# Optimization experiments

Hardware: AMD Instinct MI355X
Metric: run time of the kernel (lower is better)

Reference implementation:

```python
import jax, jax.numpy as jnp
import numpy as np


def conv1d(x, w, b):
    # x: [B, C_in, T], w: [C_out, C_in, K] (torch layout), b: [C_out]
    y = jax.lax.conv_general_dilated(
        x, w, window_strides=(1,), padding='SAME',
        dimension_numbers=('NCH', 'OIH', 'NCH'))
    return y + b[None, :, None]


def setup_inputs() -> dict:
    B, T, IN, H, D, K = 16, 2048, 80, 512, 512, 1024
    key = jax.random.key(0)
    ks = jax.random.split(key, 10)
    f32 = jnp.float32

    def w_init(k, shape, fan_in):
        return (jax.random.normal(k, shape, f32) / np.sqrt(fan_in)).astype(f32)

    return {
        'mels':    jax.random.normal(ks[0], (B, T, IN), f32),
        'enc_w1':  w_init(ks[1], (H, IN, 3), IN * 3),
        'enc_b1':  jnp.zeros((H,), f32),
        'enc_w2':  w_init(ks[2], (D, H, 3), H * 3),
        'enc_b2':  jnp.zeros((D,), f32),
        'codebook': jax.random.normal(ks[3], (K, D), f32),
        'dec_w1':  w_init(ks[4], (H, D, 3), D * 3),
        'dec_b1':  jnp.zeros((H,), f32),
        'dec_w2':  w_init(ks[5], (IN, H, 3), H * 3),
        'dec_b2':  jnp.zeros((IN,), f32),
    }


def reference(mels, enc_w1, enc_b1, enc_w2, enc_b2, codebook,
              dec_w1, dec_b1, dec_w2, dec_b2):
    B, T, _ = mels.shape
    D = codebook.shape[1]

    # ---- encoder: conv -> relu -> conv ----
    x = jnp.swapaxes(mels, 1, 2)                      # [B, in_dim, T]
    z = conv1d(jax.nn.relu(conv1d(x, enc_w1, enc_b1)), enc_w2, enc_b2)  # [B, D, T]

    # ---- vector quantization ----
    z_t = jnp.swapaxes(z, 1, 2)                       # [B, T, D]
    flat = z_t.reshape(-1, D)                         # [B*T, D]
    d = ((flat ** 2).sum(axis=1, keepdims=True)
         - 2.0 * flat @ codebook.T
         + (codebook ** 2).sum(axis=1)[None, :])      # [B*T, K]
    idx = jnp.argmin(d, axis=1).reshape(B, T)         # [B, T] int
    quantized = codebook[idx]                         # [B, T, D] gather

    # ---- decoder: conv -> relu -> conv ----
    q = jnp.swapaxes(quantized, 1, 2)                 # [B, D, T]
    recon = conv1d(jax.nn.relu(conv1d(q, dec_w1, dec_b1)), dec_w2, dec_b2)
    recon = jnp.swapaxes(recon, 1, 2)                 # [B, T, in_dim]
    return recon, idx
```

## Files before the change

### kernel.cpp

```cpp
#include <hip/hip_runtime.h>
#include <hip/hip_bf16.h>

#define Bsz   16
#define Tn    2048
#define INC   80
#define Hc    512
#define Dc    512
#define NCODE 1024
#define BT    (Bsz * Tn)
#define RECON_N (Bsz * Tn * INC)
#define MARGIN 0.03f

typedef __attribute__((ext_vector_type(8))) short bf16x8;
typedef __attribute__((ext_vector_type(4))) float f32x4;
typedef __attribute__((ext_vector_type(4))) unsigned short u16x4;

static __device__ __forceinline__ unsigned short f2bf(float x) {
    unsigned u = __float_as_uint(x);
    u += 0x7FFF + ((u >> 16) & 1);
    return (unsigned short)(u >> 16);
}
static __device__ __forceinline__ float bf2f(unsigned short h) {
    return __uint_as_float((unsigned)h << 16);
}

typedef const __attribute__((address_space(1))) unsigned int* gas_p;
typedef __attribute__((address_space(3))) unsigned int* las_p;
static __device__ __forceinline__ void async16(const void* g, const void* l) {
    __builtin_amdgcn_global_load_lds(
        (gas_p)(unsigned long long)g,
        (las_p)(unsigned int)(unsigned long long)l,
        16, 0, 0);
}

__global__ __launch_bounds__(64)
void code_norms(const float* __restrict__ CB, float* __restrict__ CN) {
    int j = blockIdx.x;
    int lane = threadIdx.x;
    const float4* row = (const float4*)(CB + (size_t)j * Dc);
    float s = 0.f;
    #pragma unroll
    for (int i = 0; i < 2; ++i) {
        float4 v = row[lane + i * 64];
        s = fmaf(v.x, v.x, s);
        s = fmaf(v.y, v.y, s);
        s = fmaf(v.z, v.z, s);
        s = fmaf(v.w, v.w, s);
    }
    #pragma unroll
    for (int off = 32; off > 0; off >>= 1) s += __shfl_down(s, off, 64);
    if (lane == 0) CN[j] = s;
}

__global__ __launch_bounds__(256)
void cb_transpose(const float* __restrict__ CB, float* __restrict__ CBt) {
    const int j0 = blockIdx.x * 64;
    const int d0 = blockIdx.y * 64;
    __shared__ float ts[64][65];
    const int tid = threadIdx.x;
    for (int i = tid; i < 4096; i += 256) {
        int r = i >> 6, c = i & 63;
        ts[r][c] = CB[(size_t)(j0 + r) * Dc + d0 + c];
    }
    __syncthreads();
    for (int i = tid; i < 4096; i += 256) {
        int r = i >> 6, c = i & 63;
        CBt[(size_t)(d0 + r) * NCODE + j0 + c] = ts[c][r];
    }
}

__global__ __launch_bounds__(256)
void mels_transpose(const float* __restrict__ M, float* __restrict__ MT) {
    const int t0 = blockIdx.x * 64;
    const int b  = blockIdx.y;
    __shared__ float ts[64][84];
    const int tid = threadIdx.x;
    #pragma unroll
    for (int it = 0; it < 5; ++it) {
        int i = tid + it * 256;
        int t = i / 20, c4 = i % 20;
        *(float4*)&ts[t][c4 * 4] =
            *(const float4*)&M[((size_t)b * Tn + t0 + t) * INC + c4 * 4];
    }
    __syncthreads();
    #pragma unroll
    for (int it = 0; it < 20; ++it) {
        int i = tid + it * 256;
        int c = i >> 6, t = i & 63;
        MT[((size_t)b * INC + c) * Tn + t0 + t] = ts[t][c];
    }
}

__global__ __launch_bounds__(256)
void wt_transpose(const float* __restrict__ W, float* __restrict__ Wt,
                  int Cin, int Cout) {
    const int o0 = blockIdx.x * 64;
    const int c0 = blockIdx.y * 16;
    __shared__ float ts[48][65];
    const int tid = threadIdx.x;
    for (int i = tid; i < 64 * 48; i += 256) {
        int o = i / 48, ck = i % 48;
        int oo = o0 + o;
        float v = 0.f;
        if (oo < Cout) v = W[(size_t)oo * Cin * 3 + c0 * 3 + ck];
        ts[ck][o] = v;
    }
    __syncthreads();
    for (int i = tid; i < 48 * 64; i += 256) {
        int o = i & 63, ck = i >> 6;
        int oo = o0 + o;
        if (oo < Cout) Wt[(size_t)(c0 * 3 + ck) * Cout + oo] = ts[ck][o];
    }
}

__global__ __launch_bounds__(256)
void wsplit(const float* __restrict__ W, unsigned short* __restrict__ Whl) {
    int o = blockIdx.x, k = blockIdx.y;
    #pragma unroll
    for (int it = 0; it < 2; ++it) {
        int c = threadIdx.x + it * 256;
        float v = W[((size_t)o * Hc + c) * 3 + k];
        unsigned short h = f2bf(v);
        size_t base = ((size_t)(k * Hc + o) * 16 + (c >> 5)) * 64 + (c & 31);
        Whl[base] = h;
        Whl[base + 32] = f2bf(v - bf2f(h));
    }
}

__global__ __launch_bounds__(256)
void wsplit80(const float* __restrict__ W, unsigned short* __restrict__ Wh) {
    int o = blockIdx.x, k = blockIdx.y;
    #pragma unroll
    for (int it = 0; it < 2; ++it) {
        int c = threadIdx.x + it * 256;
        Wh[((size_t)k * INC + o) * Hc + c] = f2bf(W[((size_t)o * Hc + c) * 3 + k]);
    }
}

__global__ __launch_bounds__(256)
void cbsplit(const float* __restrict__ CB, unsigned short* __restrict__ CBhl) {
    int j = blockIdx.x;
    #pragma unroll
    for (int it = 0; it < 2; ++it) {
        int d = threadIdx.x + it * 256;
        float v = CB[(size_t)j * Dc + d];
        unsigned short h = f2bf(v);
        size_t base = ((size_t)j * 16 + (d >> 5)) * 64 + (d & 31);
        CBhl[base] = h;
        CBhl[base + 32] = f2bf(v - bf2f(h));
    }
}

__global__ __launch_bounds__(256)
void conv_enc1(const float* __restrict__ X, const float* __restrict__ Wt,
               const float* __restrict__ bias, unsigned short* __restrict__ Yhl) {
    const int t0 = blockIdx.x * 64;
    const int o0 = blockIdx.y * 128;
    const int b  = blockIdx.z;
    union SharedU {
        struct { float Xs[16][72]; float Ws[48][132]; } a;
        float Ys[128][69];
    };
    __shared__ __align__(16) SharedU su;
    float (&Xs)[16][72]  = su.a.Xs;
    float (&Ws)[48][132] = su.a.Ws;
    const int tid = threadIdx.x;
    const int tx = tid & 15, ty = tid >> 4;
    float acc[8][4] = {};
    const float* Xb = X + (size_t)b * INC * Tn;

    for (int c0 = 0; c0 < INC; c0 += 16) {
        for (int i = tid; i < 16 * 66; i += 256) {
            int cc = i / 66, tt = i % 66;
            int t = t0 + tt - 1;
            float v = 0.f;
            if (t >= 0 && t < Tn) v = Xb[(size_t)(c0 + cc) * Tn + t];
            Xs[cc][tt] = v;
        }
        for (int i = tid; i < 48 * 128; i += 256) {
            int o = i & 127, ck = i >> 7;
            Ws[ck][o] = Wt[(size_t)(c0 * 3 + ck) * Hc + o0 + o];
        }
        __syncthreads();
        #pragma unroll
        for (int cc = 0; cc < 16; ++cc) {
            float4 xa = *(const float4*)&Xs[cc][tx * 4];
            float2 xb2 = *(const float2*)&Xs[cc][tx * 4 + 4];
            float xv[6] = {xa.x, xa.y, xa.z, xa.w, xb2.x, xb2.y};
            #pragma unroll
            for (int k = 0; k < 3; ++k) {
                float4 wa = *(const float4*)&Ws[cc * 3 + k][ty * 4];
                float4 wb = *(const float4*)&Ws[cc * 3 + k][64 + ty * 4];
                float wv[8] = {wa.x, wa.y, wa.z, wa.w, wb.x, wb.y, wb.z, wb.w};
                #pragma unroll
                for (int i8 = 0; i8 < 8; ++i8)
                    #pragma unroll
                    for (int j = 0; j < 4; ++j)
                        acc[i8][j] = fmaf(wv[i8], xv[k + j], acc[i8][j]);
            }
        }
        __syncthreads();
    }
    #pragma unroll
    for (int og = 0; og < 2; ++og)
        #pragma unroll
        for (int oi = 0; oi < 4; ++oi) {
            int ol = og * 64 + ty * 4 + oi;
            float bv = bias[o0 + ol];
            const int i8 = og * 4 + oi;
            #pragma unroll
            for (int j = 0; j < 4; ++j)
                su.Ys[ol][tx * 4 + j] = fmaxf(acc[i8][j] + bv, 0.f);
        }
    __syncthreads();
    #pragma unroll
    for (int it = 0; it < 8; ++it) {
        int i = tid + it * 256;
        int oq = i & 31, t = i >> 5;
        int o4 = o0 + oq * 4;
        u16x4 h, l;
        #pragma unroll
        for (int r = 0; r < 4; ++r) {
            float v = su.Ys[oq * 4 + r][t];
            unsigned short hh = f2bf(v);
            h[r] = hh;
            l[r] = f2bf(v - bf2f(hh));
        }
        size_t base = ((size_t)(b * (Tn + 2) + 1 + t0 + t) * 16 + (o4 >> 5)) * 64
                      + (o4 & 31);
        *(u16x4*)(Yhl + base) = h;
        *(u16x4*)(Yhl + base + 32) = l;
    }
}

__global__ __launch_bounds__(256)
void zero_guards(unsigned short* __restrict__ Yhl) {
    const int b = blockIdx.x;
    u16x4 z = {0, 0, 0, 0};
    size_t r0 = (size_t)(b * (Tn + 2)) * 1024;
    size_t r1 = (size_t)(b * (Tn + 2) + Tn + 1) * 1024;
    *(u16x4*)(Yhl + r0 + threadIdx.x * 4) = z;
    *(u16x4*)(Yhl + r1 + threadIdx.x * 4) = z;
}

__global__ __launch_bounds__(256)
void zero_guards512(unsigned short* __restrict__ Y) {
    const int b = blockIdx.x;
    u16x4 z = {0, 0, 0, 0};
    size_t r0 = (size_t)(b * (Tn + 2)) * 512;
    size_t r1 = (size_t)(b * (Tn + 2) + Tn + 1) * 512;
    if (threadIdx.x < 128) {
        *(u16x4*)(Y + r0 + threadIdx.x * 4) = z;
        *(u16x4*)(Y + r1 + threadIdx.x * 4) = z;
    }
}

__global__ __launch_bounds__(256)
void split_t(const float* __restrict__ X, unsigned short* __restrict__ Yhl,
             int rowStride, int rowOff) {
    const int t0 = blockIdx.x * 64;
    const int c0 = blockIdx.y * 64;
    const int b  = blockIdx.z;
    __shared__ __align__(16) float ts[64][68];
    const int tid = threadIdx.x;
    #pragma unroll
    for (int it = 0; it < 4; ++it) {
        int i = tid + it * 256;
        int cc = i >> 4, t4 = i & 15;
        float4 v = *(const float4*)&X[((size_t)b * Hc + c0 + cc) * Tn + t0 + t4 * 4];
        ts[t4 * 4 + 0][cc] = v.x;
        ts[t4 * 4 + 1][cc] = v.y;
        ts[t4 * 4 + 2][cc] = v.z;
        ts[t4 * 4 + 3][cc] = v.w;
    }
    __syncthreads();
    #pragma unroll
    for (int it = 0; it < 4; ++it) {
        int i = tid + it * 256;
        int t = i >> 4, c4 = i & 15;
        int c = c0 + c4 * 4;
        float4 v = *(const float4*)&ts[t][c4 * 4];
        float va[4] = {v.x, v.y, v.z, v.w};
        u16x4 h, l;
        #pragma unroll
        for (int r = 0; r < 4; ++r) {
            unsigned short hh = f2bf(va[r]);
            h[r] = hh;
            l[r] = f2bf(va[r] - bf2f(hh));
        }
        size_t base = ((size_t)(b * rowStride + rowOff + t0 + t) * 16 + (c >> 5)) * 64
                      + (c & 31);
        *(u16x4*)(Yhl + base) = h;
        *(u16x4*)(Yhl + base + 32) = l;
    }
}

__global__ __launch_bounds__(256)
void conv_mid_mfma(const unsigned short* __restrict__ Xhl,
                   const unsigned short* __restrict__ Whl,
                   const float* __restrict__ bias,
                   float* __restrict__ Y) {
    const int lin  = blockIdx.x + (blockIdx.y << 4) + (blockIdx.z << 6);
    const int slot = lin >> 3;
    const int b  = ((lin & 7) << 1) | (slot >> 6);
    const int t0 = ((slot & 63) >> 2) << 7;
    const int o0 = (slot & 3) << 7;
    __shared__ __align__(16) unsigned short XL[2][136 * 64];
    const int tid  = threadIdx.x;
    const int lane = tid & 63;
    const int wave = tid >> 6;
    const int wm = wave >> 1, wn = wave & 1;
    const int m16 = lane & 15;
    const int q = lane >> 4;
    const int lrow = lane >> 3;
    const int lchk = (lane & 7) ^ lrow;
    const unsigned short* Xb = Xhl + ((size_t)b * (Tn + 2) + t0) * 1024
                               + (size_t)lrow * 1024 + lchk * 8;

    f32x4 acc[4][4];
    #pragma unroll
    for (int mt = 0; mt < 4; ++mt)
        #pragma unroll
        for (int nt = 0; nt < 4; ++nt)
            acc[mt][nt] = (f32x4){0.f, 0.f, 0.f, 0.f};

    #pragma unroll
    for (int i = 0; i < 5; ++i) {
        int ii = wave + i * 4;
        if (ii < 17)
            async16(Xb + (size_t)ii * 8192, &XL[0][ii * 512]);
    }

    for (int c0 = 0; c0 < Hc; c0 += 32) {
        const int buf = (c0 >> 5) & 1;
        __syncthreads();
        if (c0 + 32 < Hc) {
            const unsigned short* src = Xb + (size_t)((c0 >> 5) + 1) * 64;
            #pragma unroll
            for (int i = 0; i < 5; ++i) {
                int ii = wave + i * 4;
                if (ii < 17)
                    async16(src + (size_t)ii * 8192, &XL[buf ^ 1][ii * 512]);
            }
        }
        #pragma unroll
        for (int k = 0; k < 3; ++k) {
            bf16x8 Ah[4], Al[4];
            #pragma unroll
            for (int mt = 0; mt < 4; ++mt) {
                int o = o0 + wm * 64 + mt * 16 + m16;
                size_t base = ((size_t)(k * Hc + o) * 16 + (c0 >> 5)) * 64 + q * 8;
                Ah[mt] = *(const bf16x8*)(Whl + base);
                Al[mt] = *(const bf16x8*)(Whl + base + 32);
            }
            #pragma unroll
            for (int nt = 0; nt < 4; ++nt) {
                int row = wn * 64 + nt * 16 + m16 + k;
                const unsigned short* rp = &XL[buf][row * 64];
                int ph = (q ^ (row & 7)) * 8;
                union { bf16x8 v; uint4 u; } bh, bl;
                bh.u = *(const uint4*)(rp + ph);
                bl.u = *(const uint4*)(rp + (ph ^ 32));
                __builtin_amdgcn_s_setprio(1);
                #pragma unroll
                for (int mt = 0; mt < 4; ++mt)
                    acc[mt][nt] = __builtin_amdgcn_mfma_f32_16x16x32_bf16(
                        Ah[mt], bh.v, acc[mt][nt], 0, 0, 0);
                #pragma unroll
                for (int mt = 0; mt < 4; ++mt)
                    acc[mt][nt] = __builtin_amdgcn_mfma_f32_16x16x32_bf16(
                        Al[mt], bh.v, acc[mt][nt], 0, 0, 0);
                #pragma unroll
                for (int mt = 0; mt < 4; ++mt)
                    acc[mt][nt] = __builtin_amdgcn_mfma_f32_16x16x32_bf16(
                        Ah[mt], bl.v, acc[mt][nt], 0, 0, 0);
                __builtin_amdgcn_s_setprio(0);
            }
        }
    }
    float* Yb = Y + (size_t)b * Hc * Tn;
    #pragma unroll
    for (int mt = 0; mt < 4; ++mt) {
        int ob = o0 + wm * 64 + mt * 16 + q * 4;
        float4 bq = *(const float4*)&bias[ob];
        float bqa[4] = {bq.x, bq.y, bq.z, bq.w};
        #pragma unroll
        for (int nt = 0; nt < 4; ++nt) {
            int t = t0 + wn * 64 + nt * 16 + m16;
            #pragma unroll
            for (int r = 0; r < 4; ++r)
                Yb[(size_t)(ob + r) * Tn + t] = acc[mt][nt][r] + bqa[r];
        }
    }
}

__global__ __launch_bounds__(256)
void dec2_mfma(const unsigned short* __restrict__ Xt,
               const unsigned short* __restrict__ Wh2,
               const float* __restrict__ bias, float* __restrict__ OUT) {
    const int t0 = blockIdx.x * 128;
    const int b  = blockIdx.z;
    __shared__ __align__(16) unsigned short XL[2][136 * 64];
    const int tid = threadIdx.x;
    const int lane = tid & 63;
    const int wave = tid >> 6;
    const int wn = wave;
    const int m16 = lane & 15;
    const int q = lane >> 4;
    const int lrow = lane >> 3;
    const int lchk = (lane & 7) ^ lrow;
    const unsigned short* Xb = Xt + ((size_t)b * (Tn + 2) + t0) * 512
                               + (size_t)lrow * 512 + lchk * 8;

    f32x4 acc[5][2];
    #pragma unroll
    for (int mt = 0; mt < 5; ++mt)
        #pragma unroll
        for (int nt = 0; nt < 2; ++nt)
            acc[mt][nt] = (f32x4){0.f, 0.f, 0.f, 0.f};

    #pragma unroll
    for (int i = 0; i < 5; ++i) {
        int ii = wave + i * 4;
        if (ii < 17)
            async16(Xb + (size_t)ii * 4096, &XL[0][ii * 512]);
    }

    for (int c0 = 0; c0 < Hc; c0 += 64) {
        const int buf = (c0 >> 6) & 1;
        __syncthreads();
        if (c0 + 64 < Hc) {
            const unsigned short* src = Xb + (size_t)((c0 >> 6) + 1) * 64;
            #pragma unroll
            for (int i = 0; i < 5; ++i) {
                int ii = wave + i * 4;
                if (ii < 17)
                    async16(src + (size_t)ii * 4096, &XL[buf ^ 1][ii * 512]);
            }
        }
        #pragma unroll
        for (int k = 0; k < 3; ++k) {
            #pragma unroll
            for (int sub = 0; sub < 2; ++sub) {
                int c = c0 + sub * 32;
                bf16x8 Ah[5];
                #pragma unroll
                for (int mt = 0; mt < 5; ++mt) {
                    int o = mt * 16 + m16;
                    Ah[mt] = *(const bf16x8*)(Wh2 + ((size_t)(k * INC + o)) * Hc
                                              + c + q * 8);
                }
                #pragma unroll
                for (int nt = 0; nt < 2; ++nt) {
                    int row = wn * 32 + nt * 16 + m16 + k;
                    const unsigned short* rp = &XL[buf][row * 64];
                    int p = sub * 4 + q;
                    int ph = (p ^ (row & 7)) * 8;
                    union { bf16x8 v; uint4 u; } bh;
                    bh.u = *(const uint4*)(rp + ph);
                    #pragma unroll
                    for (int mt = 0; mt < 5; ++mt)
                        acc[mt][nt] = __builtin_amdgcn_mfma_f32_16x16x32_bf16(
                            Ah[mt], bh.v, acc[mt][nt], 0, 0, 0);
                }
            }
        }
    }
    #pragma unroll
    for (int mt = 0; mt < 5; ++mt) {
        float4 bq = *(const float4*)&bias[mt * 16 + q * 4];
        #pragma unroll
        for (int nt = 0; nt < 2; ++nt) {
            int t = t0 + wn * 32 + nt * 16 + m16;
            float4 r;
            r.x = acc[mt][nt][0] + bq.x;
            r.y = acc[mt][nt][1] + bq.y;
            r.z = acc[mt][nt][2] + bq.z;
            r.w = acc[mt][nt][3] + bq.w;
            *(float4*)(OUT + ((size_t)b * Tn + t) * INC + mt * 16 + q * 4) = r;
        }
    }
}

__global__ __launch_bounds__(256)
void vq_mfma(const unsigned short* __restrict__ Zt,
             const unsigned short* __restrict__ CBhl,
             const float* __restrict__ CN,
             float* __restrict__ candv, int* __restrict__ candi,
             float* __restrict__ cand2v) {
    const int lin  = blockIdx.x + (blockIdx.y << 8);
    const int slotB = lin >> 3;
    const int nb = ((lin & 7) << 5) | (slotB & 31);
    const int jb = slotB >> 5;
    const int b  = nb >> 4;
    const int t0 = (nb & 15) * 128;
    const int jbase = jb * 128;
    __shared__ __align__(16) unsigned char pool[32768];
    unsigned short* XL0 = (unsigned short*)pool;
    unsigned short* XL1 = (unsigned short*)(pool + 16384);
    float* RV = (float*)pool;
    int*   RI = (int*)(pool + 4096);
    float* R2 = (float*)(pool + 8192);

    const int tid = threadIdx.x;
    const int lane = tid & 63;
    const int wave = tid >> 6;
    const int wm = wave >> 1, wn = wave & 1;
    const int m16 = lane & 15;
    const int q = lane >> 4;
    const int lrow = lane >> 3;
    const int lchk = (lane & 7) ^ lrow;
    const unsigned short* Zb = Zt + (size_t)(b * Tn + t0) * 1024
                               + (size_t)lrow * 1024 + lchk * 8;

    f32x4 acc[4][4];
    #pragma unroll
    for (int mt = 0; mt < 4; ++mt)
        #pragma unroll
        for (int nt = 0; nt < 4; ++nt)
            acc[mt][nt] = (f32x4){0.f, 0.f, 0.f, 0.f};

    #pragma unroll
    for (int i = 0; i < 4; ++i) {
        int ii = wave + i * 4;
        async16(Zb + (size_t)ii * 8192, XL0 + ii * 512);
    }

    for (int d0 = 0; d0 < Dc; d0 += 32) {
        const int buf = (d0 >> 5) & 1;
        unsigned short* XL = buf ? XL1 : XL0;
        __syncthreads();
        if (d0 + 32 < Dc) {
            unsigned short* XN = buf ? XL0 : XL1;
            const unsigned short* src = Zb + (size_t)((d0 >> 5) + 1) * 64;
            #pragma unroll
            for (int i = 0; i < 4; ++i) {
                int ii = wave + i * 4;
                async16(src + (size_t)ii * 8192, XN + ii * 512);
            }
        }
        bf16x8 Ah[4], Al[4];
        #pragma unroll
        for (int mt = 0; mt < 4; ++mt) {
            int j = jbase + wm * 64 + mt * 16 + m16;
            size_t base = ((size_t)j * 16 + (d0 >> 5)) * 64 + q * 8;
            Ah[mt] = *(const bf16x8*)(CBhl + base);
            Al[mt] = *(const bf16x8*)(CBhl + base + 32);
        }
        #pragma unroll
        for (int nt = 0; nt < 4; ++nt) {
            int row = wn * 64 + nt * 16 + m16;
            const unsigned short* rp = XL + row * 64;
            int ph = (q ^ (row & 7)) * 8;
            union { bf16x8 v; uint4 u; } bh, bl;
            bh.u = *(const uint4*)(rp + ph);
            bl.u = *(const uint4*)(rp + (ph ^ 32));
            __builtin_amdgcn_s_setprio(1);
            #pragma unroll
            for (int mt = 0; mt < 4; ++mt)
                acc[mt][nt] = __builtin_amdgcn_mfma_f32_16x16x32_bf16(
                    Ah[mt], bh.v, acc[mt][nt], 0, 0, 0);
            #pragma unroll
            for (int mt = 0; mt < 4; ++mt)
                acc[mt][nt] = __builtin_amdgcn_mfma_f32_16x16x32_bf16(
                    Al[mt], bh.v, acc[mt][nt], 0, 0, 0);
            #pragma unroll
            for (int mt = 0; mt < 4; ++mt)
                acc[mt][nt] = __builtin_amdgcn_mfma_f32_16x16x32_bf16(
                    Ah[mt], bl.v, acc[mt][nt], 0, 0, 0);
            __builtin_amdgcn_s_setprio(0);
        }
    }
    __syncthreads();

    float cn4[4][4];
    #pragma unroll
    for (int mt = 0; mt < 4; ++mt) {
        float4 c = *(const float4*)&CN[jbase + wm * 64 + mt * 16 + q * 4];
        cn4[mt][0] = c.x; cn4[mt][1] = c.y; cn4[mt][2] = c.z; cn4[mt][3] = c.w;
    }
    #pragma unroll
    for (int nt = 0; nt < 4; ++nt) {
        int t = wn * 64 + nt * 16 + m16;
        float v1 = 1e30f, v2 = 1e30f;
        int i1 = 0;
        #pragma unroll
        for (int mt = 0; mt < 4; ++mt)
            #pragma unroll
            for (int r = 0; r < 4; ++r) {
                float d = fmaf(-2.f, acc[mt][nt][r], cn4[mt][r]);
                int j = jbase + wm * 64 + mt * 16 + q * 4 + r;
                if (d < v1 || (d == v1 && j < i1)) { v2 = v1; v1 = d; i1 = j; }
                else if (d < v2) v2 = d;
            }
        int slotw = wm * 4 + q;
        RV[t * 8 + slotw] = v1;
        RI[t * 8 + slotw] = i1;
        R2[t * 8 + slotw] = v2;
    }
    __syncthreads();
    if (tid < 128) {
        int t = tid;
        float v1 = RV[t * 8], v2 = R2[t * 8];
        int i1 = RI[t * 8];
        #pragma unroll
        for (int s = 1; s < 8; ++s) {
            float a1 = RV[t * 8 + s], a2 = R2[t * 8 + s];
            int ai = RI[t * 8 + s];
            if (a1 < v1 || (a1 == v1 && ai < i1)) {
                v2 = fminf(v1, a2); v1 = a1; i1 = ai;
            } else {
                v2 = fminf(v2, a1);
            }
        }
        int n = b * Tn + t0 + t;
        candv[(size_t)jb * BT + n] = v1;
        candi[(size_t)jb * BT + n] = i1;
        cand2v[(size_t)jb * BT + n] = v2;
    }
}

__global__ __launch_bounds__(256)
void vq_reduce2(const float* __restrict__ candv, const int* __restrict__ candi,
                const float* __restrict__ cand2v, int* __restrict__ idxI,
                float* __restrict__ idxf, int* __restrict__ flagn,
                int* __restrict__ flaglist) {
    int n = blockIdx.x * 256 + threadIdx.x;
    float v1 = candv[n], v2 = cand2v[n];
    int i1 = candi[n];
    #pragma unroll
    for (int jq = 1; jq < 8; ++jq) {
        float a1 = candv[(size_t)jq * BT + n];
        float a2 = cand2v[(size_t)jq * BT + n];
        int ai = candi[(size_t)jq * BT + n];
        if (a1 < v1 || (a1 == v1 && ai < i1)) {
            v2 = fminf(v1, a2); v1 = a1; i1 = ai;
        } else {
            v2 = fminf(v2, a1);
        }
    }
    idxI[n] = i1;
    idxf[n] = (float)i1;
    if (v2 - v1 < MARGIN) {
        int s = atomicAdd(flagn, 1);
        flaglist[s] = n;
    }
}

__global__ __launch_bounds__(256)
void vq_rescue(const int* __restrict__ flagn, const int* __restrict__ flaglist,
               const float* __restrict__ Z, const float* __restrict__ CB,
               const float* __restrict__ CN, int* __restrict__ idxI,
               float* __restrict__ idxf) {
    __shared__ float zs[512];
    __shared__ float rvv[256];
    __shared__ int   rii[256];
    const int nf = *flagn;
    for (int f = blockIdx.x; f < nf; f += gridDim.x) {
        int n = flaglist[f];
        int b = n / Tn, t = n - b * Tn;
        __syncthreads();
        #pragma unroll
        for (int it = 0; it < 2; ++it) {
            int d = threadIdx.x + it * 256;
            zs[d] = Z[((size_t)b * Dc + d) * Tn + t];
        }
        __syncthreads();
        float bv = 1e30f;
        int bi = 0;
        #pragma unroll
        for (int jj = 0; jj < 4; ++jj) {
            int j = threadIdx.x * 4 + jj;
            const float* cr = CB + (size_t)j * Dc;
            float dot = 0.f;
            for (int d = 0; d < Dc; ++d) dot = fmaf(zs[d], cr[d], dot);
            float dist = fmaf(-2.f, dot, CN[j]);
            if (dist < bv || (dist == bv && j < bi)) { bv = dist; bi = j; }
        }
        rvv[threadIdx.x] = bv;
        rii[threadIdx.x] = bi;
        __syncthreads();
        for (int off = 128; off > 0; off >>= 1) {
            if (threadIdx.x < off) {
                float ov = rvv[threadIdx.x + off];
                int oi = rii[threadIdx.x + off];
                if (ov < rvv[threadIdx.x] ||
                    (ov == rvv[threadIdx.x] && oi < rii[threadIdx.x])) {
                    rvv[threadIdx.x] = ov; rii[threadIdx.x] = oi;
                }
            }
            __syncthreads();
        }
        if (threadIdx.x == 0) {
            idxI[n] = rii[0];
            idxf[n] = (float)rii[0];
        }
    }
}

__global__ __launch_bounds__(256)
void gemm_g(const float* __restrict__ CBt, const float* __restrict__ Wt,
            float* __restrict__ G) {
    const int j0 = blockIdx.x * 64;
    const int kk = blockIdx.y >> 2;
    const int o0 = (blockIdx.y & 3) * 128;
    __shared__ __align__(16) float As[16][68];
    __shared__ __align__(16) float Bs[16][132];
    const int tid = threadIdx.x;
    const int tx = tid & 15, ty = tid >> 4;
    float acc[4][8] = {};

    for (int c0 = 0; c0 < Dc; c0 += 16) {
        {
            int cc = tid >> 4, j4 = tid & 15;
            *(float4*)&As[cc][j4 * 4] =
                *(const float4*)&CBt[(size_t)(c0 + cc) * NCODE + j0 + j4 * 4];
        }
        #pragma unroll
        for (int it = 0; it < 2; ++it) {
            int i = tid + it * 256;
            int cc = i >> 5, o4 = i & 31;
            *(float4*)&Bs[cc][o4 * 4] =
                *(const float4*)&Wt[(size_t)((c0 + cc) * 3 + kk) * Hc + o0 + o4 * 4];
        }
        __syncthreads();
        #pragma unroll
        for (int cc = 0; cc < 16; ++cc) {
            float4 a = *(const float4*)&As[cc][tx * 4];
            float av[4] = {a.x, a.y, a.z, a.w};
            float4 b0 = *(const float4*)&Bs[cc][ty * 4];
            float4 b1 = *(const float4*)&Bs[cc][64 + ty * 4];
            float bv[8] = {b0.x, b0.y, b0.z, b0.w, b1.x, b1.y, b1.z, b1.w};
            #pragma unroll
            for (int jj = 0; jj < 4; ++jj)
                #pragma unroll
                for (int oo = 0; oo < 8; ++oo)
                    acc[jj][oo] = fmaf(av[jj], bv[oo], acc[jj][oo]);
        }
        __syncthreads();
    }
    #pragma unroll
    for (int jj = 0; jj < 4; ++jj) {
        int j = j0 + tx * 4 + jj;
        float* gp = G + (size_t)j * 1536 + kk * 512 + o0;
        *(float4*)(gp + ty * 4) = *(float4*)&acc[jj][0];
        *(float4*)(gp + 64 + ty * 4) = *(float4*)&acc[jj][4];
    }
}

__global__ __launch_bounds__(256)
void dec_y3(const int* __restrict__ idx, const float* __restrict__ G,
            const float* __restrict__ bias, unsigned short* __restrict__ Yt) {
    const int t0 = blockIdx.x * 64;
    const int o0 = blockIdx.y * 128;
    const int b  = blockIdx.z;
    const int tid = threadIdx.x;
    __shared__ int sidx[66];
    __shared__ __align__(16) float Ys[128][68];

    if (tid < 66) {
        int t = t0 + tid - 1;
        sidx[tid] = (t >= 0 && t < Tn) ? idx[b * Tn + t] : -1;
    }
    __syncthreads();

    const int o = tid & 127;
    const int half = tid >> 7;
    float acc[32] = {};
    #pragma unroll
    for (int kk = 0; kk < 3; ++kk) {
        const float* Gk = G + (size_t)kk * 512 + o0 + o;
        #pragma unroll
        for (int k = 0; k < 32; ++k) {
            int j = sidx[half + 2 * k + kk];
            if (j >= 0) acc[k] += Gk[(size_t)j * 1536];
        }
    }
    float bv = bias[o0 + o];
    #pragma unroll
    for (int k = 0; k < 32; ++k)
        Ys[o][half + 2 * k] = fmaxf(acc[k] + bv, 0.f);
    __syncthreads();

    unsigned short* Yb = Yt + ((size_t)(b * (Tn + 2) + 1 + t0)) * 512 + o0;
    #pragma unroll
    for (int it = 0; it < 8; ++it) {
        int i = tid + it * 256;
        int t = i >> 5, oq = i & 31;
        u16x4 h;
        #pragma unroll
        for (int r = 0; r < 4; ++r)
            h[r] = f2bf(Ys[oq * 4 + r][t]);
        *(u16x4*)(Yb + (size_t)t * 512 + oq * 4) = h;
    }
}

extern "C" void kernel_launch(void* const* d_in, const int* in_sizes, int n_in,
                              void* d_out, int out_size, void* d_ws, size_t ws_size,
                              hipStream_t stream) {
    const float* mels    = (const float*)d_in[0];
    const float* enc_w1  = (const float*)d_in[1];
    const float* enc_b1  = (const float*)d_in[2];
    const float* enc_w2  = (const float*)d_in[3];
    const float* enc_b2  = (const float*)d_in[4];
    const float* codebook= (const float*)d_in[5];
    const float* dec_w1  = (const float*)d_in[6];
    const float* dec_b1  = (const float*)d_in[7];
    const float* dec_w2  = (const float*)d_in[8];
    const float* dec_b2  = (const float*)d_in[9];

    float* out = (float*)d_out;
    float* recon = out;
    float* idxf  = out + RECON_N;

    const size_t ACT = (size_t)Bsz * Hc * Tn;
    const size_t Y1HL_U = (size_t)Bsz * (Tn + 2) * 1024 + 16384;
    const size_t R2F = Y1HL_U / 2;

    float* zf = (float*)d_ws;
    unsigned short* y3t = (unsigned short*)d_ws;
    float* r2 = (float*)d_ws + ACT;
    unsigned short* y1hl = (unsigned short*)r2;
    unsigned short* Zt   = (unsigned short*)r2;
    float* sm    = r2 + R2F;
    int*   idxI  = (int*)sm;
    float* cn    = (float*)(idxI + BT);
    float* cbt   = cn + NCODE;
    float* wt1   = cbt + (size_t)Dc * NCODE;
    float* wt3   = wt1 + (size_t)INC * 3 * Hc;
    float* candv = wt3 + (size_t)Dc * 3 * Hc;
    float* cand2v= candv + (size_t)8 * BT;
    int*   candi = (int*)(cand2v + (size_t)8 * BT);
    int*   flagn = candi + (size_t)8 * BT;
    int*   flaglist = flagn + 4;
    float* G     = (float*)(flaglist + BT);
    unsigned short* whl  = (unsigned short*)(G + (size_t)NCODE * 1536);
    unsigned short* cbhl = whl + (size_t)3 * Hc * 1024;
    unsigned short* wh2  = cbhl + (size_t)NCODE * 1024;
    float* melsT = (float*)(wh2 + (size_t)3 * INC * Hc);

    dim3 blk(256);
    hipMemsetAsync(flagn, 0, 16, stream);
    code_norms<<<dim3(NCODE), dim3(64), 0, stream>>>(codebook, cn);
    cb_transpose<<<dim3(NCODE / 64, Dc / 64), blk, 0, stream>>>(codebook, cbt);
    mels_transpose<<<dim3(Tn / 64, Bsz), blk, 0, stream>>>(mels, melsT);
    wt_transpose<<<dim3(Hc / 64, INC / 16), blk, 0, stream>>>(enc_w1, wt1, INC, Hc);
    wsplit<<<dim3(Hc, 3), blk, 0, stream>>>(enc_w2, whl);
    cbsplit<<<dim3(NCODE), blk, 0, stream>>>(codebook, cbhl);
    wt_transpose<<<dim3(Hc / 64, Dc / 16), blk, 0, stream>>>(dec_w1, wt3, Dc, Hc);
    wsplit80<<<dim3(INC, 3), blk, 0, stream>>>(dec_w2, wh2);
    gemm_g<<<dim3(NCODE / 64, 12), blk, 0, stream>>>(cbt, wt3, G);
    zero_guards<<<dim3(Bsz), blk, 0, stream>>>(y1hl);
    conv_enc1<<<dim3(Tn / 64, Hc / 128, Bsz), blk, 0, stream>>>(melsT, wt1, enc_b1,
                                                                y1hl);
    conv_mid_mfma<<<dim3(Tn / 128, Hc / 128, Bsz), blk, 0, stream>>>(y1hl, whl,
                                                                     enc_b2, zf);
    split_t<<<dim3(Tn / 64, Hc / 64, Bsz), blk, 0, stream>>>(zf, Zt, Tn, 0);
    vq_mfma<<<dim3(BT / 128, NCODE / 128), blk, 0, stream>>>(Zt, cbhl, cn,
                                                             candv, candi, cand2v);
    vq_reduce2<<<dim3(BT / 256), blk, 0, stream>>>(candv, candi, cand2v, idxI,
                                                   idxf, flagn, flaglist);
    vq_rescue<<<dim3(128), blk, 0, stream>>>(flagn, flaglist, zf, codebook, cn,
                                             idxI, idxf);
    zero_guards512<<<dim3(Bsz), blk, 0, stream>>>(y3t);
    dec_y3<<<dim3(Tn / 64, 4, Bsz), blk, 0, stream>>>(idxI, G, dec_b1, y3t);
    dec2_mfma<<<dim3(Tn / 128, 1, Bsz), blk, 0, stream>>>(y3t, wh2, dec_b2, recon);
}
```

Before: 793.7 us.

## Fuse bf16 hi/lo split into conv epilogue and fold guard zeroing into producers

The encoder's second conv now writes its output directly in the transposed bf16 hi/lo layout used by the VQ matmul, plus a third bf16 residual term stored separately. This removes the fp32 activation write, the separate split_t transpose kernel, and the fp32 re-read. The rescue path rebuilds near-exact z from the three bf16 parts instead of reading fp32. The guard-row zeroing kernels are dropped, and their work is done inside the edge blocks of conv_enc1 and dec_y3, which saves two launches. The cost is strided 8-byte scattered stores from the MFMA epilogue and a reconstructed rather than exact fp32 z in rescue.

```diff
diff --git a/kernel.cpp b/kernel.cpp
--- a/kernel.cpp
+++ b/kernel.cpp
@@ -169,6 +169,16 @@
     float acc[8][4] = {};
     const float* Xb = X + (size_t)b * INC * Tn;
 
+    if (blockIdx.x == 0 && tid < 64) {
+        u16x4 z4 = {0, 0, 0, 0};
+        *(u16x4*)(Yhl + ((size_t)(b * (Tn + 2)) * 16 + (o0 >> 5)) * 64 + tid * 4) = z4;
+    }
+    if (blockIdx.x == Tn / 64 - 1 && tid < 64) {
+        u16x4 z4 = {0, 0, 0, 0};
+        *(u16x4*)(Yhl + ((size_t)(b * (Tn + 2) + Tn + 1) * 16 + (o0 >> 5)) * 64
+                  + tid * 4) = z4;
+    }
+
     for (int c0 = 0; c0 < INC; c0 += 16) {
         for (int i = tid; i < 16 * 66; i += 256) {
             int cc = i / 66, tt = i % 66;
@@ -234,72 +244,11 @@
 }
 
 __global__ __launch_bounds__(256)
-void zero_guards(unsigned short* __restrict__ Yhl) {
-    const int b = blockIdx.x;
-    u16x4 z = {0, 0, 0, 0};
-    size_t r0 = (size_t)(b * (Tn + 2)) * 1024;
-    size_t r1 = (size_t)(b * (Tn + 2) + Tn + 1) * 1024;
-    *(u16x4*)(Yhl + r0 + threadIdx.x * 4) = z;
-    *(u16x4*)(Yhl + r1 + threadIdx.x * 4) = z;
-}
-
-__global__ __launch_bounds__(256)
-void zero_guards512(unsigned short* __restrict__ Y) {
-    const int b = blockIdx.x;
-    u16x4 z = {0, 0, 0, 0};
-    size_t r0 = (size_t)(b * (Tn + 2)) * 512;
-    size_t r1 = (size_t)(b * (Tn + 2) + Tn + 1) * 512;
-    if (threadIdx.x < 128) {
-        *(u16x4*)(Y + r0 + threadIdx.x * 4) = z;
-        *(u16x4*)(Y + r1 + threadIdx.x * 4) = z;
-    }
-}
-
-__global__ __launch_bounds__(256)
-void split_t(const float* __restrict__ X, unsigned short* __restrict__ Yhl,
-             int rowStride, int rowOff) {
-    const int t0 = blockIdx.x * 64;
-    const int c0 = blockIdx.y * 64;
-    const int b  = blockIdx.z;
-    __shared__ __align__(16) float ts[64][68];
-    const int tid = threadIdx.x;
-    #pragma unroll
-    for (int it = 0; it < 4; ++it) {
-        int i = tid + it * 256;
-        int cc = i >> 4, t4 = i & 15;
-        float4 v = *(const float4*)&X[((size_t)b * Hc + c0 + cc) * Tn + t0 + t4 * 4];
-        ts[t4 * 4 + 0][cc] = v.x;
-        ts[t4 * 4 + 1][cc] = v.y;
-        ts[t4 * 4 + 2][cc] = v.z;
-        ts[t4 * 4 + 3][cc] = v.w;
-    }
-    __syncthreads();
-    #pragma unroll
-    for (int it = 0; it < 4; ++it) {
-        int i = tid + it * 256;
-        int t = i >> 4, c4 = i & 15;
-        int c = c0 + c4 * 4;
-        float4 v = *(const float4*)&ts[t][c4 * 4];
-        float va[4] = {v.x, v.y, v.z, v.w};
-        u16x4 h, l;
-        #pragma unroll
-        for (int r = 0; r < 4; ++r) {
-            unsigned short hh = f2bf(va[r]);
-            h[r] = hh;
-            l[r] = f2bf(va[r] - bf2f(hh));
-        }
-        size_t base = ((size_t)(b * rowStride + rowOff + t0 + t) * 16 + (c >> 5)) * 64
-                      + (c & 31);
-        *(u16x4*)(Yhl + base) = h;
-        *(u16x4*)(Yhl + base + 32) = l;
-    }
-}
-
-__global__ __launch_bounds__(256)
 void conv_mid_mfma(const unsigned short* __restrict__ Xhl,
                    const unsigned short* __restrict__ Whl,
                    const float* __restrict__ bias,
-                   float* __restrict__ Y) {
+                   unsigned short* __restrict__ Zt,
+                   unsigned short* __restrict__ Lo2) {
     const int lin  = blockIdx.x + (blockIdx.y << 4) + (blockIdx.z << 6);
     const int slot = lin >> 3;
     const int b  = ((lin & 7) << 1) | (slot >> 6);
@@ -378,7 +327,7 @@
             }
         }
     }
-    float* Yb = Y + (size_t)b * Hc * Tn;
+    unsigned short* Lb = Lo2 + (size_t)b * Tn * 512;
     #pragma unroll
     for (int mt = 0; mt < 4; ++mt) {
         int ob = o0 + wm * 64 + mt * 16 + q * 4;
@@ -387,9 +336,21 @@
         #pragma unroll
         for (int nt = 0; nt < 4; ++nt) {
             int t = t0 + wn * 64 + nt * 16 + m16;
-            #pragma unroll
-            for (int r = 0; r < 4; ++r)
-                Yb[(size_t)(ob + r) * Tn + t] = acc[mt][nt][r] + bqa[r];
+            u16x4 h, l, l2;
+            #pragma unroll
+            for (int r = 0; r < 4; ++r) {
+                float v = acc[mt][nt][r] + bqa[r];
+                unsigned short hh = f2bf(v);
+                float r1 = v - bf2f(hh);
+                unsigned short ll = f2bf(r1);
+                h[r] = hh;
+                l[r] = ll;
+                l2[r] = f2bf(r1 - bf2f(ll));
+            }
+            size_t zb = ((size_t)(b * Tn + t) * 16 + (ob >> 5)) * 64 + (ob & 31);
+            *(u16x4*)(Zt + zb) = h;
+            *(u16x4*)(Zt + zb + 32) = l;
+            *(u16x4*)(Lb + (size_t)t * 512 + ob) = l2;
         }
     }
 }
@@ -649,7 +610,9 @@
 
 __global__ __launch_bounds__(256)
 void vq_rescue(const int* __restrict__ flagn, const int* __restrict__ flaglist,
-               const float* __restrict__ Z, const float* __restrict__ CB,
+               const unsigned short* __restrict__ Zt,
+               const unsigned short* __restrict__ Lo2,
+               const float* __restrict__ CB,
                const float* __restrict__ CN, int* __restrict__ idxI,
                float* __restrict__ idxf) {
     __shared__ float zs[512];
@@ -658,12 +621,13 @@
     const int nf = *flagn;
     for (int f = blockIdx.x; f < nf; f += gridDim.x) {
         int n = flaglist[f];
-        int b = n / Tn, t = n - b * Tn;
         __syncthreads();
         #pragma unroll
         for (int it = 0; it < 2; ++it) {
             int d = threadIdx.x + it * 256;
-            zs[d] = Z[((size_t)b * Dc + d) * Tn + t];
+            const unsigned short* zr = Zt + ((size_t)n * 16 + (d >> 5)) * 64
+                                       + (d & 31);
+            zs[d] = bf2f(zr[0]) + bf2f(zr[32]) + bf2f(Lo2[(size_t)n * 512 + d]);
         }
         __syncthreads();
         float bv = 1e30f;
@@ -757,6 +721,15 @@
     const int tid = threadIdx.x;
     __shared__ int sidx[66];
     __shared__ __align__(16) float Ys[128][68];
+
+    if (blockIdx.x == 0 && tid < 32) {
+        u16x4 z4 = {0, 0, 0, 0};
+        *(u16x4*)(Yt + (size_t)(b * (Tn + 2)) * 512 + o0 + tid * 4) = z4;
+    }
+    if (blockIdx.x == Tn / 64 - 1 && tid < 32) {
+        u16x4 z4 = {0, 0, 0, 0};
+        *(u16x4*)(Yt + (size_t)(b * (Tn + 2) + Tn + 1) * 512 + o0 + tid * 4) = z4;
+    }
 
     if (tid < 66) {
         int t = t0 + tid - 1;
@@ -817,11 +790,10 @@
     const size_t Y1HL_U = (size_t)Bsz * (Tn + 2) * 1024 + 16384;
     const size_t R2F = Y1HL_U / 2;
 
-    float* zf = (float*)d_ws;
+    unsigned short* Zt  = (unsigned short*)d_ws;
     unsigned short* y3t = (unsigned short*)d_ws;
     float* r2 = (float*)d_ws + ACT;
     unsigned short* y1hl = (unsigned short*)r2;
-    unsigned short* Zt   = (unsigned short*)r2;
     float* sm    = r2 + R2F;
     int*   idxI  = (int*)sm;
     float* cn    = (float*)(idxI + BT);
@@ -838,6 +810,7 @@
     unsigned short* cbhl = whl + (size_t)3 * Hc * 1024;
     unsigned short* wh2  = cbhl + (size_t)NCODE * 1024;
     float* melsT = (float*)(wh2 + (size_t)3 * INC * Hc);
+    unsigned short* lo2 = (unsigned short*)melsT;
 
     dim3 blk(256);
     hipMemsetAsync(flagn, 0, 16, stream);
@@ -850,19 +823,17 @@
     wt_transpose<<<dim3(Hc / 64, Dc / 16), blk, 0, stream>>>(dec_w1, wt3, Dc, Hc);
     wsplit80<<<dim3(INC, 3), blk, 0, stream>>>(dec_w2, wh2);
     gemm_g<<<dim3(NCODE / 64, 12), blk, 0, stream>>>(cbt, wt3, G);
-    zero_guards<<<dim3(Bsz), blk, 0, stream>>>(y1hl);
     conv_enc1<<<dim3(Tn / 64, Hc / 128, Bsz), blk, 0, stream>>>(melsT, wt1, enc_b1,
                                                                 y1hl);
     conv_mid_mfma<<<dim3(Tn / 128, Hc / 128, Bsz), blk, 0, stream>>>(y1hl, whl,
-                                                                     enc_b2, zf);
-    split_t<<<dim3(Tn / 64, Hc / 64, Bsz), blk, 0, stream>>>(zf, Zt, Tn, 0);
+                                                                     enc_b2,
+                                                                     Zt, lo2);
     vq_mfma<<<dim3(BT / 128, NCODE / 128), blk, 0, stream>>>(Zt, cbhl, cn,
                                                              candv, candi, cand2v);
     vq_reduce2<<<dim3(BT / 256), blk, 0, stream>>>(candv, candi, cand2v, idxI,
                                                    idxf, flagn, flaglist);
-    vq_rescue<<<dim3(128), blk, 0, stream>>>(flagn, flaglist, zf, codebook, cn,
-                                             idxI, idxf);
-    zero_guards512<<<dim3(Bsz), blk, 0, stream>>>(y3t);
+    vq_rescue<<<dim3(128), blk, 0, stream>>>(flagn, flaglist, Zt, lo2, codebook,
+                                             cn, idxI, idxf);
     dec_y3<<<dim3(Tn / 64, 4, Bsz), blk, 0, stream>>>(idxI, G, dec_b1, y3t);
     dec2_mfma<<<dim3(Tn / 128, 1, Bsz), blk, 0, stream>>>(y3t, wh2, dec_b2, recon);
 }
```

Measured after the change: 790.6 us. No clear change (-0.4%).
